# Performance work log

Hardware: AMD Instinct MI355X
Metric: run time of the kernel (lower is better)

Reference implementation:

```python
import jax, jax.numpy as jnp
import numpy as np

L, D, H, E, K, HID = 4096, 1024, 16, 8, 2, 4096
HEAD_DIM = D // H
SCALE = 1.0 / np.sqrt(HEAD_DIM)


def setup_inputs() -> dict:
    key = jax.random.key(0)
    ks = jax.random.split(key, 9)
    s = 0.02
    return {
        "Q": jax.random.normal(ks[0], (L, D), dtype=jnp.float32),
        "K": jax.random.normal(ks[1], (L, D), dtype=jnp.float32),
        "V": jax.random.normal(ks[2], (L, D), dtype=jnp.float32),
        "gate_w": jax.random.normal(ks[3], (D, E), dtype=jnp.float32) * s,
        "w1": jax.random.normal(ks[4], (E, D, HID), dtype=jnp.float32) * s,
        "b1": jnp.zeros((E, HID), dtype=jnp.float32),
        "w2": jax.random.normal(ks[5], (E, HID, D), dtype=jnp.float32) * s,
        "b2": jnp.zeros((E, D), dtype=jnp.float32),
    }


def attention(Q, Kt, V):
    # [L, D] -> [L, H, head_dim]
    q = Q.reshape(L, H, HEAD_DIM)
    k = Kt.reshape(L, H, HEAD_DIM)
    v = V.reshape(L, H, HEAD_DIM)
    scores = jnp.einsum("qhd,khd->hqk", q, k) * SCALE  # [H, L, L]
    probs = jax.nn.softmax(scores, axis=-1)
    out = jnp.einsum("hqk,khd->qhd", probs, v)  # [L, H, head_dim]
    return out.reshape(L, D)


def moe(x, gate_w, w1, b1, w2, b2):
    # x: [N, D]; top-k gating with softmax over selected logits
    logits = x @ gate_w  # [N, E]
    topv, topi = jax.lax.top_k(logits, K)  # [N, K]
    topw = jax.nn.softmax(topv, axis=-1)
    rows = jnp.arange(x.shape[0])[:, None]
    full_w = jnp.zeros_like(logits).at[rows, topi].set(topw)  # [N, E]
    # dense-masked expert compute (mathematically identical: zero weights kill
    # unrouted tokens). GELU is exact (erf), matching torch nn.GELU default.
    h = jax.nn.gelu(jnp.einsum("nd,edh->enh", x, w1) + b1[:, None, :],
                    approximate=False)  # [E, N, HID]
    y = jnp.einsum("enh,ehd->end", h, w2) + b2[:, None, :]  # [E, N, D]
    return jnp.einsum("ne,end->nd", full_w, y)  # weighted combine


def reference(Q, K, V, gate_w, w1, b1, w2, b2):
    attn_out = attention(Q, K, V)              # [L, D]
    out = moe(attn_out, gate_w, w1, b1, w2, b2)  # [L, D]
    return out
```

## Files before the change

kernel.cpp:

```cpp
#include <hip/hip_runtime.h>
#include <hip/hip_bf16.h>
#include <math.h>

#define L_SEQ 4096
#define DMODEL 1024
#define NHEAD 16
#define HDIM 64
#define NEXP 8
#define NHID 4096
#define NSLOT (L_SEQ * 2)

typedef __attribute__((ext_vector_type(4))) float f32x4;
typedef __attribute__((ext_vector_type(16))) float f32x16;
typedef __attribute__((ext_vector_type(8))) short s16x8;
typedef __attribute__((ext_vector_type(4))) short s16x4;
typedef __attribute__((ext_vector_type(4))) unsigned u32x4;

__device__ __forceinline__ short f2bf(float f) {
  __hip_bfloat16 h = __float2bfloat16(f);
  return *reinterpret_cast<short*>(&h);
}
__device__ __forceinline__ float bf2f(short s) {
  __hip_bfloat16 h;
  *reinterpret_cast<short*>(&h) = s;
  return __bfloat162float(h);
}
__device__ __forceinline__ void split3(float a, short& h, short& m, short& l) {
  h = f2bf(a);
  float r = a - bf2f(h);
  m = f2bf(r);
  float r2 = r - bf2f(m);
  l = f2bf(r2);
}
__device__ __forceinline__ void gload16(const void* g, void* l) {
  __builtin_amdgcn_global_load_lds(
      (const __attribute__((address_space(1))) void*)g,
      (__attribute__((address_space(3))) void*)l, 16, 0, 0);
}

__global__ __launch_bounds__(256) void split_kernel(const float* __restrict__ src,
                                                    short* __restrict__ hs,
                                                    short* __restrict__ ms,
                                                    short* __restrict__ ls,
                                                    float scale, int nquad) {
  int i = blockIdx.x * 256 + threadIdx.x;
  for (; i < nquad; i += gridDim.x * 256) {
    f32x4 a = reinterpret_cast<const f32x4*>(src)[i];
    a *= scale;
    s16x4 h4, m4, l4;
    #pragma unroll
    for (int j = 0; j < 4; ++j) {
      short h, m, l;
      split3(a[j], h, m, l);
      h4[j] = h; m4[j] = m; l4[j] = l;
    }
    reinterpret_cast<s16x4*>(hs)[i] = h4;
    reinterpret_cast<s16x4*>(ms)[i] = m4;
    reinterpret_cast<s16x4*>(ls)[i] = l4;
  }
}

__global__ __launch_bounds__(256) void split_vt_kernel(const float* __restrict__ V,
                                                       short* __restrict__ Vth,
                                                       short* __restrict__ Vtm,
                                                       short* __restrict__ Vtl) {
  __shared__ float Vlds[64][65];
  const int k0 = blockIdx.x * 64;
  const int head = blockIdx.y;
  const int t = threadIdx.x;
  {
    int r = t >> 2, c = (t & 3) * 16;
    const f32x4* src = reinterpret_cast<const f32x4*>(&V[(size_t)(k0 + r) * DMODEL + head * HDIM + c]);
    #pragma unroll
    for (int j = 0; j < 4; ++j)
      *reinterpret_cast<f32x4*>(&Vlds[r][c + 4 * j]) = src[j];
  }
  __syncthreads();
  {
    int d = t >> 2, kc = (t & 3) * 16;
    s16x8 h8[2], m8[2], l8[2];
    #pragma unroll
    for (int j = 0; j < 16; ++j) {
      float v = Vlds[kc + j][d];
      short h, m, l;
      split3(v, h, m, l);
      h8[j >> 3][j & 7] = h; m8[j >> 3][j & 7] = m; l8[j >> 3][j & 7] = l;
    }
    size_t base = (size_t)(head * HDIM + d) * L_SEQ + k0 + kc;
    *reinterpret_cast<s16x8*>(&Vth[base]) = h8[0];
    *reinterpret_cast<s16x8*>(&Vth[base + 8]) = h8[1];
    *reinterpret_cast<s16x8*>(&Vtm[base]) = m8[0];
    *reinterpret_cast<s16x8*>(&Vtm[base + 8]) = m8[1];
    *reinterpret_cast<s16x8*>(&Vtl[base]) = l8[0];
    *reinterpret_cast<s16x8*>(&Vtl[base + 8]) = l8[1];
  }
}

__global__ __launch_bounds__(256) void wtrans_kernel(const float* __restrict__ src,
                                                     short* __restrict__ dst,
                                                     int R, int C) {
  __shared__ float T[64][65];
  const int e = blockIdx.z;
  const int r0 = blockIdx.y * 64, c0 = blockIdx.x * 64;
  const size_t sbase = (size_t)e * R * C;
  const int t = threadIdx.x;
  {
    int rr = t >> 2, cc = (t & 3) * 16;
    #pragma unroll
    for (int j = 0; j < 4; ++j)
      *reinterpret_cast<f32x4*>(&T[rr][cc + 4 * j]) =
          *reinterpret_cast<const f32x4*>(&src[sbase + (size_t)(r0 + rr) * C + c0 + cc + 4 * j]);
  }
  __syncthreads();
  {
    int c = t >> 2, r = (t & 3) * 16;
    s16x8 v0, v1;
    #pragma unroll
    for (int j = 0; j < 8; ++j) { v0[j] = f2bf(T[r + j][c]); v1[j] = f2bf(T[r + 8 + j][c]); }
    size_t dbase = ((size_t)e * C + c0 + c) * R + r0 + r;
    *reinterpret_cast<s16x8*>(&dst[dbase]) = v0;
    *reinterpret_cast<s16x8*>(&dst[dbase + 8]) = v1;
  }
}

__global__ __launch_bounds__(256, 2) void attn_mfma(
    const short* __restrict__ Qh, const short* __restrict__ Qm, const short* __restrict__ Ql,
    const short* __restrict__ Kh, const short* __restrict__ Km, const short* __restrict__ Kl,
    const short* __restrict__ Vth, const short* __restrict__ Vtm, const short* __restrict__ Vtl,
    float* __restrict__ X, short* __restrict__ Xb) {
  __shared__ short Ks[3][64][70];
  __shared__ short Vs[3][64][70];
  const int lin = blockIdx.x;
  const int swz = (lin & 7) * 64 + (lin >> 3);
  const int head = swz >> 5;
  const int q0 = (swz & 31) << 7;
  const int t = threadIdx.x;
  const int l = t & 63;
  const int wq = t >> 6;
  const int lc = l & 31;
  const int hh = l >> 5;

  const short* Qp[3] = {Qh, Qm, Ql};
  const short* Kp[3] = {Kh, Km, Kl};
  const short* Vp[3] = {Vth, Vtm, Vtl};

  s16x8 qf[3][4];
  {
    size_t qrow = (size_t)(q0 + wq * 32 + lc) * DMODEL + head * HDIM;
    #pragma unroll
    for (int s = 0; s < 3; ++s)
      #pragma unroll
      for (int ds_ = 0; ds_ < 4; ++ds_)
        qf[s][ds_] = *reinterpret_cast<const s16x8*>(&Qp[s][qrow + ds_ * 16 + hh * 8]);
  }

  s16x8 sK[3][2], sV[3][2];
  const int c0 = t * 2;
  const int row0 = c0 >> 3, ch0 = (c0 & 7) * 8;
  const int row1 = (c0 + 1) >> 3, ch1 = ((c0 + 1) & 7) * 8;

  #define LOAD_TILE(k0v)                                                                  \
    _Pragma("unroll")                                                                     \
    for (int s = 0; s < 3; ++s) {                                                         \
      sK[s][0] = *reinterpret_cast<const s16x8*>(&Kp[s][(size_t)((k0v) + row0) * DMODEL + head * HDIM + ch0]); \
      sK[s][1] = *reinterpret_cast<const s16x8*>(&Kp[s][(size_t)((k0v) + row1) * DMODEL + head * HDIM + ch1]); \
      sV[s][0] = *reinterpret_cast<const s16x8*>(&Vp[s][(size_t)(head * HDIM + row0) * L_SEQ + (k0v) + ch0]);  \
      sV[s][1] = *reinterpret_cast<const s16x8*>(&Vp[s][(size_t)(head * HDIM + row1) * L_SEQ + (k0v) + ch1]);  \
    }

  f32x16 acc0 = (f32x16)0.f, acc1 = (f32x16)0.f;
  float l_loc = 0.f;
  const float LOG2E = 1.4426950408889634f;
  const float MBIAS = 46.166241f;

  LOAD_TILE(0);

  for (int kt64 = 0; kt64 < 64; ++kt64) {
    __syncthreads();
    #pragma unroll
    for (int s = 0; s < 3; ++s) {
      *reinterpret_cast<s16x8*>(&Ks[s][row0][ch0]) = sK[s][0];
      *reinterpret_cast<s16x8*>(&Ks[s][row1][ch1]) = sK[s][1];
      *reinterpret_cast<s16x8*>(&Vs[s][row0][ch0]) = sV[s][0];
      *reinterpret_cast<s16x8*>(&Vs[s][row1][ch1]) = sV[s][1];
    }
    __syncthreads();
    if (kt64 < 63) { LOAD_TILE((kt64 + 1) * 64); }

    #pragma unroll
    for (int khalf = 0; khalf < 2; ++khalf) {
      f32x16 st = (f32x16)0.f;
      #pragma unroll
      for (int ds_ = 0; ds_ < 4; ++ds_) {
        s16x8 ah = *reinterpret_cast<const s16x8*>(&Ks[0][khalf * 32 + lc][ds_ * 16 + hh * 8]);
        s16x8 am = *reinterpret_cast<const s16x8*>(&Ks[1][khalf * 32 + lc][ds_ * 16 + hh * 8]);
        s16x8 al = *reinterpret_cast<const s16x8*>(&Ks[2][khalf * 32 + lc][ds_ * 16 + hh * 8]);
        st = __builtin_amdgcn_mfma_f32_32x32x16_bf16(am, qf[1][ds_], st, 0, 0, 0);
        st = __builtin_amdgcn_mfma_f32_32x32x16_bf16(al, qf[0][ds_], st, 0, 0, 0);
        st = __builtin_amdgcn_mfma_f32_32x32x16_bf16(ah, qf[2][ds_], st, 0, 0, 0);
        st = __builtin_amdgcn_mfma_f32_32x32x16_bf16(am, qf[0][ds_], st, 0, 0, 0);
        st = __builtin_amdgcn_mfma_f32_32x32x16_bf16(ah, qf[1][ds_], st, 0, 0, 0);
        st = __builtin_amdgcn_mfma_f32_32x32x16_bf16(ah, qf[0][ds_], st, 0, 0, 0);
      }

      unsigned Eh[4][2], Em[4][2], El[4][2];
      float ps = 0.f;
      #pragma unroll
      for (int q = 0; q < 4; ++q) {
        #pragma unroll
        for (int p = 0; p < 2; ++p) {
          float a = exp2f(fmaf(st[4 * q + 2 * p],     LOG2E, -MBIAS));
          float b = exp2f(fmaf(st[4 * q + 2 * p + 1], LOG2E, -MBIAS));
          ps += a + b;
          unsigned ua = __float_as_uint(a), ub = __float_as_uint(b);
          unsigned ha = ua & 0xffff0000u, hb = ub & 0xffff0000u;
          Eh[q][p] = (ha >> 16) | hb;
          float ra = a - __uint_as_float(ha), rb = b - __uint_as_float(hb);
          unsigned ma = __float_as_uint(ra) & 0xffff0000u, mb = __float_as_uint(rb) & 0xffff0000u;
          Em[q][p] = (ma >> 16) | mb;
          float la = ra - __uint_as_float(ma), lb = rb - __uint_as_float(mb);
          El[q][p] = ((__float_as_uint(la) & 0xffff0000u) >> 16) | (__float_as_uint(lb) & 0xffff0000u);
        }
      }
      l_loc += ps;

      #define EXCH(E, Fout) do { u32x4 f_;                                        \
        _Pragma("unroll") for (int p_ = 0; p_ < 2; ++p_) {                        \
          unsigned sel_ = hh ? E[2 * ks][p_] : E[2 * ks + 1][p_];                 \
          unsigned rc_ = (unsigned)__shfl_xor((int)sel_, 32);                     \
          f_[p_] = hh ? rc_ : E[2 * ks][p_];                                      \
          f_[2 + p_] = hh ? E[2 * ks + 1][p_] : rc_;                              \
        }                                                                         \
        Fout = *reinterpret_cast<s16x8*>(&f_); } while (0)

      #pragma unroll
      for (int ks = 0; ks < 2; ++ks) {
        s16x8 Fh, Fm, Fl;
        EXCH(Eh, Fh);
        EXCH(Em, Fm);
        EXCH(El, Fl);
        const int kcol = khalf * 32 + ks * 16 + hh * 8;
        {
          s16x8 vh = *reinterpret_cast<const s16x8*>(&Vs[0][lc][kcol]);
          s16x8 vm = *reinterpret_cast<const s16x8*>(&Vs[1][lc][kcol]);
          s16x8 vl = *reinterpret_cast<const s16x8*>(&Vs[2][lc][kcol]);
          acc0 = __builtin_amdgcn_mfma_f32_32x32x16_bf16(Fm, vm, acc0, 0, 0, 0);
          acc0 = __builtin_amdgcn_mfma_f32_32x32x16_bf16(Fl, vh, acc0, 0, 0, 0);
          acc0 = __builtin_amdgcn_mfma_f32_32x32x16_bf16(Fh, vl, acc0, 0, 0, 0);
          acc0 = __builtin_amdgcn_mfma_f32_32x32x16_bf16(Fm, vh, acc0, 0, 0, 0);
          acc0 = __builtin_amdgcn_mfma_f32_32x32x16_bf16(Fh, vm, acc0, 0, 0, 0);
          acc0 = __builtin_amdgcn_mfma_f32_32x32x16_bf16(Fh, vh, acc0, 0, 0, 0);
        }
        {
          s16x8 vh = *reinterpret_cast<const s16x8*>(&Vs[0][32 + lc][kcol]);
          s16x8 vm = *reinterpret_cast<const s16x8*>(&Vs[1][32 + lc][kcol]);
          s16x8 vl = *reinterpret_cast<const s16x8*>(&Vs[2][32 + lc][kcol]);
          acc1 = __builtin_amdgcn_mfma_f32_32x32x16_bf16(Fm, vm, acc1, 0, 0, 0);
          acc1 = __builtin_amdgcn_mfma_f32_32x32x16_bf16(Fl, vh, acc1, 0, 0, 0);
          acc1 = __builtin_amdgcn_mfma_f32_32x32x16_bf16(Fh, vl, acc1, 0, 0, 0);
          acc1 = __builtin_amdgcn_mfma_f32_32x32x16_bf16(Fm, vh, acc1, 0, 0, 0);
          acc1 = __builtin_amdgcn_mfma_f32_32x32x16_bf16(Fh, vm, acc1, 0, 0, 0);
          acc1 = __builtin_amdgcn_mfma_f32_32x32x16_bf16(Fh, vh, acc1, 0, 0, 0);
        }
      }
      #undef EXCH
    }
  }

  float l_tot = l_loc + __shfl_xor(l_loc, 32);
  float inv = 1.f / l_tot;
  #pragma unroll
  for (int r = 0; r < 16; ++r) {
    int qrow_ = (r & 3) + 8 * (r >> 2) + 4 * hh;
    float invr = __int_as_float(__builtin_amdgcn_ds_bpermute(qrow_ << 2, __float_as_int(inv)));
    size_t base = (size_t)(q0 + wq * 32 + qrow_) * DMODEL + head * HDIM + lc;
    float o0 = acc0[r] * invr, o1 = acc1[r] * invr;
    X[base] = o0;
    X[base + 32] = o1;
    Xb[base] = f2bf(o0);
    Xb[base + 32] = f2bf(o1);
  }
}

__global__ __launch_bounds__(256) void gate_kernel(const float* __restrict__ X,
                                                   const float* __restrict__ GW,
                                                   int* __restrict__ tokE,
                                                   float* __restrict__ tokW,
                                                   int* __restrict__ meta) {
  const int gid = blockIdx.x * 256 + threadIdx.x;
  const int n = gid >> 6;
  const int lane = threadIdx.x & 63;
  double lacc[8];
  #pragma unroll
  for (int e = 0; e < 8; ++e) lacc[e] = 0.0;
  #pragma unroll
  for (int ch = 0; ch < 4; ++ch) {
    int d0 = ch * 256 + lane * 4;
    f32x4 xv = *reinterpret_cast<const f32x4*>(&X[(size_t)n * DMODEL + d0]);
    #pragma unroll
    for (int j = 0; j < 4; ++j) {
      const f32x4* g = reinterpret_cast<const f32x4*>(&GW[(size_t)(d0 + j) * 8]);
      f32x4 g0 = g[0], g1 = g[1];
      double xd = (double)xv[j];
      lacc[0] += xd * (double)g0[0]; lacc[1] += xd * (double)g0[1];
      lacc[2] += xd * (double)g0[2]; lacc[3] += xd * (double)g0[3];
      lacc[4] += xd * (double)g1[0]; lacc[5] += xd * (double)g1[1];
      lacc[6] += xd * (double)g1[2]; lacc[7] += xd * (double)g1[3];
    }
  }
  #pragma unroll
  for (int e = 0; e < 8; ++e) {
    double v = lacc[e];
    #pragma unroll
    for (int off = 32; off > 0; off >>= 1) v += __shfl_down(v, off);
    lacc[e] = v;
  }
  if (lane == 0) {
    float lg[8];
    #pragma unroll
    for (int e = 0; e < 8; ++e) lg[e] = (float)lacc[e];
    int i0 = 0;
    for (int e = 1; e < 8; ++e) if (lg[e] > lg[i0]) i0 = e;
    int i1 = -1;
    for (int e = 0; e < 8; ++e) {
      if (e == i0) continue;
      if (i1 < 0 || lg[e] > lg[i1]) i1 = e;
    }
    float eb = expf(lg[i1] - lg[i0]);
    float wa = 1.f / (1.f + eb);
    float wb = eb * wa;
    tokE[2 * n] = i0; tokE[2 * n + 1] = i1;
    tokW[2 * n] = wa; tokW[2 * n + 1] = wb;
    atomicAdd(&meta[i0], 1);
    atomicAdd(&meta[i1], 1);
  }
}

__global__ void scan_kernel(int* meta) {
  if (threadIdx.x == 0) {
    int s = 0;
    for (int e = 0; e < 8; ++e) { meta[8 + e] = s; meta[16 + e] = s; s += meta[e]; }
  }
}

__global__ __launch_bounds__(256) void assign_kernel(const int* __restrict__ tokE,
                                                     const float* __restrict__ tokW,
                                                     int* __restrict__ meta,
                                                     int* __restrict__ list,
                                                     float* __restrict__ wl) {
  int n = blockIdx.x * 256 + threadIdx.x;
  if (n >= L_SEQ) return;
  #pragma unroll
  for (int k2 = 0; k2 < 2; ++k2) {
    int e = tokE[2 * n + k2];
    int slot = atomicAdd(&meta[16 + e], 1);
    list[slot] = n;
    wl[slot] = tokW[2 * n + k2];
  }
}

__global__ __launch_bounds__(256) void gemm1p_kernel(const short* __restrict__ Xb,
                                                     const short* __restrict__ W1t,
                                                     const float* __restrict__ B1,
                                                     const int* __restrict__ meta,
                                                     const int* __restrict__ list,
                                                     short* __restrict__ Hb) {
  const int e = blockIdx.z;
  const int cntE = meta[e];
  const int flat = blockIdx.x + gridDim.x * blockIdx.y;
  const int xcd = flat & 7;
  const int idx = flat >> 3;
  const int m0 = (idx & 31) << 7;
  const int n0 = ((xcd << 2) + (idx >> 5)) << 7;
  if (m0 >= cntE) return;
  const int baseE = meta[8 + e];

  __shared__ short As[3][128 * 32];
  __shared__ short Bs[3][128 * 32];

  const int t = threadIdx.x;
  const int l = t & 63;
  const int w = t >> 6;
  const int wm = w >> 1, wn = w & 1;
  const int ln = l & 15, kg = l >> 4;

  size_t asrc[2], bsrc[2];
  #pragma unroll
  for (int c = 0; c < 2; ++c) {
    int idx2 = c * 256 + t;
    int row = idx2 >> 2;
    int sch = (idx2 & 3) ^ ((row >> 2) & 3);
    int idxm = m0 + row; if (idxm > cntE - 1) idxm = cntE - 1;
    int grow = list[baseE + idxm];
    asrc[c] = ((size_t)grow * DMODEL + sch * 8) * 2;
    bsrc[c] = (((size_t)e * NHID + n0 + row) * DMODEL + sch * 8) * 2;
  }

  f32x4 acc[4][4];
  #pragma unroll
  for (int mi = 0; mi < 4; ++mi)
    #pragma unroll
    for (int ni = 0; ni < 4; ++ni) acc[mi][ni] = (f32x4)0.f;

  #define STG1(h_, bf_) do { size_t ko_ = (size_t)(h_) * 64;                        \
    _Pragma("unroll")                                                               \
    for (int c_ = 0; c_ < 2; ++c_) {                                                \
      gload16((const char*)Xb + asrc[c_] + ko_, (char*)As + (bf_) * 8192 + c_ * 4096 + t * 16);  \
      gload16((const char*)W1t + bsrc[c_] + ko_, (char*)Bs + (bf_) * 8192 + c_ * 4096 + t * 16); \
    } } while (0)

  const int H = DMODEL / 32;
  STG1(0, 0); STG1(1, 1);
  for (int h = 0; h < H; ++h) {
    if (h < H - 1) asm volatile("s_waitcnt vmcnt(4)\ns_barrier" ::: "memory");
    else           asm volatile("s_waitcnt vmcnt(0)\ns_barrier" ::: "memory");
    if (h + 2 < H) STG1(h + 2, (h + 2) % 3);
    const char* ab = (const char*)As + (h % 3) * 8192;
    const char* bb = (const char*)Bs + (h % 3) * 8192;
    s16x8 af[4];
    #pragma unroll
    for (int mi = 0; mi < 4; ++mi) {
      int row = wm * 64 + mi * 16 + ln;
      int cc = kg ^ ((row >> 2) & 3);
      af[mi] = *reinterpret_cast<const s16x8*>(ab + row * 64 + cc * 16);
    }
    #pragma unroll
    for (int ni = 0; ni < 4; ++ni) {
      int col = wn * 64 + ni * 16 + ln;
      int cc = kg ^ ((col >> 2) & 3);
      s16x8 bfr = *reinterpret_cast<const s16x8*>(bb + col * 64 + cc * 16);
      #pragma unroll
      for (int mi = 0; mi < 4; ++mi)
        acc[mi][ni] = __builtin_amdgcn_mfma_f32_16x16x32_bf16(af[mi], bfr, acc[mi][ni], 0, 0, 0);
    }
  }

  #pragma unroll
  for (int mi = 0; mi < 4; ++mi) {
    #pragma unroll
    for (int r = 0; r < 4; ++r) {
      int rl = wm * 64 + mi * 16 + kg * 4 + r;
      if (m0 + rl >= cntE) continue;
      size_t hrow = (size_t)(baseE + m0 + rl) * NHID;
      #pragma unroll
      for (int ni = 0; ni < 4; ++ni) {
        int col = n0 + wn * 64 + ni * 16 + ln;
        float z = acc[mi][ni][r] + B1[e * NHID + col];
        float g = 0.5f * z * (1.f + erff(z * 0.70710678118f));
        Hb[hrow + col] = f2bf(g);
      }
    }
  }
}

__global__ __launch_bounds__(256) void gemm2p_kernel(const short* __restrict__ Hb,
                                                     const short* __restrict__ W2t,
                                                     const float* __restrict__ B2,
                                                     const int* __restrict__ meta,
                                                     const int* __restrict__ list,
                                                     const float* __restrict__ wl,
                                                     float* __restrict__ out) {
  const int e = blockIdx.z;
  const int cntE = meta[e];
  const int flat = blockIdx.x + gridDim.x * blockIdx.y;
  const int m0 = (flat >> 3) << 7;
  const int n0 = (flat & 7) << 7;
  if (m0 >= cntE) return;
  const int baseE = meta[8 + e];

  __shared__ short As[3][128 * 32];
  __shared__ short Bs[3][128 * 32];

  const int t = threadIdx.x;
  const int l = t & 63;
  const int w = t >> 6;
  const int wm = w >> 1, wn = w & 1;
  const int ln = l & 15, kg = l >> 4;

  size_t asrc[2], bsrc[2];
  #pragma unroll
  for (int c = 0; c < 2; ++c) {
    int idx2 = c * 256 + t;
    int row = idx2 >> 2;
    int sch = (idx2 & 3) ^ ((row >> 2) & 3);
    int idxm = m0 + row; if (idxm > cntE - 1) idxm = cntE - 1;
    asrc[c] = (((size_t)(baseE + idxm)) * NHID + sch * 8) * 2;
    bsrc[c] = (((size_t)e * DMODEL + n0 + row) * NHID + sch * 8) * 2;
  }

  f32x4 acc[4][4];
  #pragma unroll
  for (int mi = 0; mi < 4; ++mi)
    #pragma unroll
    for (int ni = 0; ni < 4; ++ni) acc[mi][ni] = (f32x4)0.f;

  #define STG2(h_, bf_) do { size_t ko_ = (size_t)(h_) * 64;                        \
    _Pragma("unroll")                                                               \
    for (int c_ = 0; c_ < 2; ++c_) {                                                \
      gload16((const char*)Hb + asrc[c_] + ko_, (char*)As + (bf_) * 8192 + c_ * 4096 + t * 16);  \
      gload16((const char*)W2t + bsrc[c_] + ko_, (char*)Bs + (bf_) * 8192 + c_ * 4096 + t * 16); \
    } } while (0)

  const int H = NHID / 32;
  STG2(0, 0); STG2(1, 1);
  for (int h = 0; h < H; ++h) {
    if (h < H - 1) asm volatile("s_waitcnt vmcnt(4)\ns_barrier" ::: "memory");
    else           asm volatile("s_waitcnt vmcnt(0)\ns_barrier" ::: "memory");
    if (h + 2 < H) STG2(h + 2, (h + 2) % 3);
    const char* ab = (const char*)As + (h % 3) * 8192;
    const char* bb = (const char*)Bs + (h % 3) * 8192;
    s16x8 af[4];
    #pragma unroll
    for (int mi = 0; mi < 4; ++mi) {
      int row = wm * 64 + mi * 16 + ln;
      int cc = kg ^ ((row >> 2) & 3);
      af[mi] = *reinterpret_cast<const s16x8*>(ab + row * 64 + cc * 16);
    }
    #pragma unroll
    for (int ni = 0; ni < 4; ++ni) {
      int col = wn * 64 + ni * 16 + ln;
      int cc = kg ^ ((col >> 2) & 3);
      s16x8 bfr = *reinterpret_cast<const s16x8*>(bb + col * 64 + cc * 16);
      #pragma unroll
      for (int mi = 0; mi < 4; ++mi)
        acc[mi][ni] = __builtin_amdgcn_mfma_f32_16x16x32_bf16(af[mi], bfr, acc[mi][ni], 0, 0, 0);
    }
  }

  #pragma unroll
  for (int mi = 0; mi < 4; ++mi) {
    #pragma unroll
    for (int r = 0; r < 4; ++r) {
      int rl = wm * 64 + mi * 16 + kg * 4 + r;
      if (m0 + rl >= cntE) continue;
      int slot = baseE + m0 + rl;
      int token = list[slot];
      float wgt = wl[slot];
      #pragma unroll
      for (int ni = 0; ni < 4; ++ni) {
        int col = n0 + wn * 64 + ni * 16 + ln;
        float z = acc[mi][ni][r] + B2[e * DMODEL + col];
        atomicAdd(&out[(size_t)token * DMODEL + col], wgt * z);
      }
    }
  }
}

extern "C" void kernel_launch(void* const* d_in, const int* in_sizes, int n_in,
                              void* d_out, int out_size, void* d_ws, size_t ws_size,
                              hipStream_t stream) {
  const float* Q  = (const float*)d_in[0];
  const float* K  = (const float*)d_in[1];
  const float* V  = (const float*)d_in[2];
  const float* GW = (const float*)d_in[3];
  const float* W1 = (const float*)d_in[4];
  const float* B1 = (const float*)d_in[5];
  const float* W2 = (const float*)d_in[6];
  const float* B2 = (const float*)d_in[7];
  float* out = (float*)d_out;

  const size_t SPLIT = (size_t)L_SEQ * DMODEL;
  const size_t WT_BYTES = (size_t)NEXP * NHID * DMODEL * 2;
  const size_t SPLIT_REGION = SPLIT * 2 * 9;
  const size_t SMALL = (size_t)L_SEQ * 2 * 4 * 2 + (size_t)NSLOT * 4 * 2 + 256;
  const size_t PRIMARY_BYTES = WT_BYTES * 2 + SPLIT_REGION + SPLIT * 4 + SPLIT * 2 + SMALL;
  if (ws_size < PRIMARY_BYTES) return;

  char* ws = (char*)d_ws;
  const int nquad = (int)(SPLIT / 4);

  size_t off = 0;
  short* W1t = (short*)(ws + off); off += WT_BYTES;
  short* W2t = (short*)(ws + off); off += WT_BYTES;
  char*  splits = ws + off;        off += SPLIT_REGION;
  short* Qh = (short*)(splits);
  short* Qm = Qh + SPLIT;  short* Ql = Qm + SPLIT;
  short* Kh = Ql + SPLIT;  short* Km = Kh + SPLIT;  short* Kl = Km + SPLIT;
  short* Vth = Kl + SPLIT; short* Vtm = Vth + SPLIT; short* Vtl = Vtm + SPLIT;
  short* Hb = (short*)splits;
  float* Xf = (float*)(ws + off);  off += SPLIT * 4;
  short* Xb = (short*)(ws + off);  off += SPLIT * 2;
  int*   tokE = (int*)(ws + off);  off += (size_t)L_SEQ * 2 * 4;
  float* tokW = (float*)(ws + off); off += (size_t)L_SEQ * 2 * 4;
  int*   list = (int*)(ws + off);  off += (size_t)NSLOT * 4;
  float* wl = (float*)(ws + off);  off += (size_t)NSLOT * 4;
  int*   meta = (int*)(ws + off);  off += 256;

  hipMemsetAsync(out, 0, (size_t)out_size * sizeof(float), stream);
  hipMemsetAsync(meta, 0, 256, stream);

  wtrans_kernel<<<dim3(64, 16, 8), 256, 0, stream>>>(W1, W1t, DMODEL, NHID);
  wtrans_kernel<<<dim3(16, 64, 8), 256, 0, stream>>>(W2, W2t, NHID, DMODEL);
  split_kernel<<<dim3(2048), 256, 0, stream>>>(Q, Qh, Qm, Ql, 0.125f, nquad);
  split_kernel<<<dim3(2048), 256, 0, stream>>>(K, Kh, Km, Kl, 1.0f, nquad);
  split_vt_kernel<<<dim3(64, 16), 256, 0, stream>>>(V, Vth, Vtm, Vtl);
  attn_mfma<<<dim3(512), 256, 0, stream>>>(Qh, Qm, Ql, Kh, Km, Kl, Vth, Vtm, Vtl, Xf, Xb);
  gate_kernel<<<dim3(1024), 256, 0, stream>>>(Xf, GW, tokE, tokW, meta);
  scan_kernel<<<1, 64, 0, stream>>>(meta);
  assign_kernel<<<dim3(16), 256, 0, stream>>>(tokE, tokW, meta, list, wl);
  gemm1p_kernel<<<dim3(32, 32, 8), 256, 0, stream>>>(Xb, W1t, B1, meta, list, Hb);
  gemm2p_kernel<<<dim3(32, 8, 8), 256, 0, stream>>>(Hb, W2t, B2, meta, list, wl, out);
}
```

Measured before the change: 992.3 us.

## Fuse prep kernels, compact MoE grids via tile maps, enlarge GEMM1 M-tile

Result: slower. 1.105 ms (+11.3%).

```diff
diff --git a/kernel.cpp b/kernel.cpp
--- a/kernel.cpp
+++ b/kernel.cpp
@@ -38,70 +38,82 @@
       (__attribute__((address_space(3))) void*)l, 16, 0, 0);
 }
 
-__global__ __launch_bounds__(256) void split_kernel(const float* __restrict__ src,
-                                                    short* __restrict__ hs,
-                                                    short* __restrict__ ms,
-                                                    short* __restrict__ ls,
-                                                    float scale, int nquad) {
-  int i = blockIdx.x * 256 + threadIdx.x;
-  for (; i < nquad; i += gridDim.x * 256) {
-    f32x4 a = reinterpret_cast<const f32x4*>(src)[i];
-    a *= scale;
-    s16x4 h4, m4, l4;
-    #pragma unroll
-    for (int j = 0; j < 4; ++j) {
-      short h, m, l;
-      split3(a[j], h, m, l);
-      h4[j] = h; m4[j] = m; l4[j] = l;
-    }
-    reinterpret_cast<s16x4*>(hs)[i] = h4;
-    reinterpret_cast<s16x4*>(ms)[i] = m4;
-    reinterpret_cast<s16x4*>(ls)[i] = l4;
-  }
-}
-
-__global__ __launch_bounds__(256) void split_vt_kernel(const float* __restrict__ V,
-                                                       short* __restrict__ Vth,
-                                                       short* __restrict__ Vtm,
-                                                       short* __restrict__ Vtl) {
+__global__ __launch_bounds__(256) void prep_kernel(
+    const float* __restrict__ Q, const float* __restrict__ K, const float* __restrict__ V,
+    short* __restrict__ Qh, short* __restrict__ Qm, short* __restrict__ Ql,
+    short* __restrict__ Kh, short* __restrict__ Km, short* __restrict__ Kl,
+    short* __restrict__ Vth, short* __restrict__ Vtm, short* __restrict__ Vtl) {
   __shared__ float Vlds[64][65];
-  const int k0 = blockIdx.x * 64;
-  const int head = blockIdx.y;
+  const int b = blockIdx.x;
   const int t = threadIdx.x;
-  {
-    int r = t >> 2, c = (t & 3) * 16;
-    const f32x4* src = reinterpret_cast<const f32x4*>(&V[(size_t)(k0 + r) * DMODEL + head * HDIM + c]);
-    #pragma unroll
-    for (int j = 0; j < 4; ++j)
-      *reinterpret_cast<f32x4*>(&Vlds[r][c + 4 * j]) = src[j];
-  }
-  __syncthreads();
-  {
-    int d = t >> 2, kc = (t & 3) * 16;
-    s16x8 h8[2], m8[2], l8[2];
-    #pragma unroll
-    for (int j = 0; j < 16; ++j) {
-      float v = Vlds[kc + j][d];
-      short h, m, l;
-      split3(v, h, m, l);
-      h8[j >> 3][j & 7] = h; m8[j >> 3][j & 7] = m; l8[j >> 3][j & 7] = l;
-    }
-    size_t base = (size_t)(head * HDIM + d) * L_SEQ + k0 + kc;
-    *reinterpret_cast<s16x8*>(&Vth[base]) = h8[0];
-    *reinterpret_cast<s16x8*>(&Vth[base + 8]) = h8[1];
-    *reinterpret_cast<s16x8*>(&Vtm[base]) = m8[0];
-    *reinterpret_cast<s16x8*>(&Vtm[base + 8]) = m8[1];
-    *reinterpret_cast<s16x8*>(&Vtl[base]) = l8[0];
-    *reinterpret_cast<s16x8*>(&Vtl[base + 8]) = l8[1];
-  }
-}
-
-__global__ __launch_bounds__(256) void wtrans_kernel(const float* __restrict__ src,
-                                                     short* __restrict__ dst,
-                                                     int R, int C) {
+  if (b < 4096) {
+    const bool isQ = (b < 2048);
+    const float* src = isQ ? Q : K;
+    short* hs = isQ ? Qh : Kh;
+    short* ms = isQ ? Qm : Km;
+    short* ls = isQ ? Ql : Kl;
+    const float scale = isQ ? 0.125f : 1.0f;
+    const int nquad = (int)((size_t)L_SEQ * DMODEL / 4);
+    int i = (b & 2047) * 256 + t;
+    for (; i < nquad; i += 2048 * 256) {
+      f32x4 a = reinterpret_cast<const f32x4*>(src)[i];
+      a *= scale;
+      s16x4 h4, m4, l4;
+      #pragma unroll
+      for (int j = 0; j < 4; ++j) {
+        short h, m, l;
+        split3(a[j], h, m, l);
+        h4[j] = h; m4[j] = m; l4[j] = l;
+      }
+      reinterpret_cast<s16x4*>(hs)[i] = h4;
+      reinterpret_cast<s16x4*>(ms)[i] = m4;
+      reinterpret_cast<s16x4*>(ls)[i] = l4;
+    }
+  } else {
+    const int b2 = b - 4096;
+    const int k0 = (b2 & 63) * 64;
+    const int head = b2 >> 6;
+    {
+      int r = t >> 2, c = (t & 3) * 16;
+      const f32x4* src = reinterpret_cast<const f32x4*>(&V[(size_t)(k0 + r) * DMODEL + head * HDIM + c]);
+      #pragma unroll
+      for (int j = 0; j < 4; ++j)
+        *reinterpret_cast<f32x4*>(&Vlds[r][c + 4 * j]) = src[j];
+    }
+    __syncthreads();
+    {
+      int d = t >> 2, kc = (t & 3) * 16;
+      s16x8 h8[2], m8[2], l8[2];
+      #pragma unroll
+      for (int j = 0; j < 16; ++j) {
+        float v = Vlds[kc + j][d];
+        short h, m, l;
+        split3(v, h, m, l);
+        h8[j >> 3][j & 7] = h; m8[j >> 3][j & 7] = m; l8[j >> 3][j & 7] = l;
+      }
+      size_t base = (size_t)(head * HDIM + d) * L_SEQ + k0 + kc;
+      *reinterpret_cast<s16x8*>(&Vth[base]) = h8[0];
+      *reinterpret_cast<s16x8*>(&Vth[base + 8]) = h8[1];
+      *reinterpret_cast<s16x8*>(&Vtm[base]) = m8[0];
+      *reinterpret_cast<s16x8*>(&Vtm[base + 8]) = m8[1];
+      *reinterpret_cast<s16x8*>(&Vtl[base]) = l8[0];
+      *reinterpret_cast<s16x8*>(&Vtl[base + 8]) = l8[1];
+    }
+  }
+}
+
+__global__ __launch_bounds__(256) void wtrans_kernel(const float* __restrict__ W1,
+                                                     const float* __restrict__ W2,
+                                                     short* __restrict__ W1t,
+                                                     short* __restrict__ W2t) {
   __shared__ float T[64][65];
-  const int e = blockIdx.z;
-  const int r0 = blockIdx.y * 64, c0 = blockIdx.x * 64;
+  const int f = blockIdx.x;
+  const int z = blockIdx.y;
+  const float* src;
+  short* dst;
+  int R, C, r0, c0, e;
+  if (z < 8) { e = z; R = DMODEL; C = NHID; src = W1; dst = W1t; r0 = (f >> 6) * 64; c0 = (f & 63) * 64; }
+  else { e = z - 8; R = NHID; C = DMODEL; src = W2; dst = W2t; r0 = (f >> 4) * 64; c0 = (f & 15) * 64; }
   const size_t sbase = (size_t)e * R * C;
   const int t = threadIdx.x;
   {
@@ -336,10 +348,18 @@
   }
 }
 
-__global__ void scan_kernel(int* meta) {
+__global__ void scan_kernel(int* meta, int* map1, int* map2) {
   if (threadIdx.x == 0) {
-    int s = 0;
-    for (int e = 0; e < 8; ++e) { meta[8 + e] = s; meta[16 + e] = s; s += meta[e]; }
+    int s = 0, c1 = 0, c2 = 0;
+    for (int e = 0; e < 8; ++e) {
+      meta[8 + e] = s; meta[16 + e] = s;
+      int cnt = meta[e];
+      for (int m0 = 0; m0 < cnt; m0 += 256) { map1[2 * c1] = e; map1[2 * c1 + 1] = m0; ++c1; }
+      for (int m0 = 0; m0 < cnt; m0 += 128) { map2[2 * c2] = e; map2[2 * c2 + 1] = m0; ++c2; }
+      s += cnt;
+    }
+    for (; c1 < 64; ++c1) map1[2 * c1] = -1;
+    for (; c2 < 80; ++c2) map2[2 * c2] = -1;
   }
 }
 
@@ -359,23 +379,21 @@
   }
 }
 
-__global__ __launch_bounds__(256) void gemm1p_kernel(const short* __restrict__ Xb,
-                                                     const short* __restrict__ W1t,
-                                                     const float* __restrict__ B1,
-                                                     const int* __restrict__ meta,
-                                                     const int* __restrict__ list,
-                                                     short* __restrict__ Hb) {
-  const int e = blockIdx.z;
+__global__ __launch_bounds__(256, 2) void gemm1p_kernel(const short* __restrict__ Xb,
+                                                        const short* __restrict__ W1t,
+                                                        const float* __restrict__ B1,
+                                                        const int* __restrict__ meta,
+                                                        const int* __restrict__ list,
+                                                        const int* __restrict__ map1,
+                                                        short* __restrict__ Hb) {
+  const int e = map1[2 * blockIdx.x];
+  if (e < 0) return;
+  const int m0 = map1[2 * blockIdx.x + 1];
+  const int n0 = blockIdx.y << 7;
   const int cntE = meta[e];
-  const int flat = blockIdx.x + gridDim.x * blockIdx.y;
-  const int xcd = flat & 7;
-  const int idx = flat >> 3;
-  const int m0 = (idx & 31) << 7;
-  const int n0 = ((xcd << 2) + (idx >> 5)) << 7;
-  if (m0 >= cntE) return;
   const int baseE = meta[8 + e];
 
-  __shared__ short As[3][128 * 32];
+  __shared__ short As[3][256 * 32];
   __shared__ short Bs[3][128 * 32];
 
   const int t = threadIdx.x;
@@ -384,62 +402,70 @@
   const int wm = w >> 1, wn = w & 1;
   const int ln = l & 15, kg = l >> 4;
 
-  size_t asrc[2], bsrc[2];
-  #pragma unroll
-  for (int c = 0; c < 2; ++c) {
+  size_t asrc[4], bsrc[2];
+  #pragma unroll
+  for (int c = 0; c < 4; ++c) {
     int idx2 = c * 256 + t;
     int row = idx2 >> 2;
     int sch = (idx2 & 3) ^ ((row >> 2) & 3);
     int idxm = m0 + row; if (idxm > cntE - 1) idxm = cntE - 1;
     int grow = list[baseE + idxm];
     asrc[c] = ((size_t)grow * DMODEL + sch * 8) * 2;
+  }
+  #pragma unroll
+  for (int c = 0; c < 2; ++c) {
+    int idx2 = c * 256 + t;
+    int row = idx2 >> 2;
+    int sch = (idx2 & 3) ^ ((row >> 2) & 3);
     bsrc[c] = (((size_t)e * NHID + n0 + row) * DMODEL + sch * 8) * 2;
   }
 
-  f32x4 acc[4][4];
-  #pragma unroll
-  for (int mi = 0; mi < 4; ++mi)
+  f32x4 acc[8][4];
+  #pragma unroll
+  for (int mi = 0; mi < 8; ++mi)
     #pragma unroll
     for (int ni = 0; ni < 4; ++ni) acc[mi][ni] = (f32x4)0.f;
 
   #define STG1(h_, bf_) do { size_t ko_ = (size_t)(h_) * 64;                        \
     _Pragma("unroll")                                                               \
-    for (int c_ = 0; c_ < 2; ++c_) {                                                \
-      gload16((const char*)Xb + asrc[c_] + ko_, (char*)As + (bf_) * 8192 + c_ * 4096 + t * 16);  \
+    for (int c_ = 0; c_ < 4; ++c_)                                                  \
+      gload16((const char*)Xb + asrc[c_] + ko_, (char*)As + (bf_) * 16384 + c_ * 4096 + t * 16); \
+    _Pragma("unroll")                                                               \
+    for (int c_ = 0; c_ < 2; ++c_)                                                  \
       gload16((const char*)W1t + bsrc[c_] + ko_, (char*)Bs + (bf_) * 8192 + c_ * 4096 + t * 16); \
-    } } while (0)
+    } while (0)
 
   const int H = DMODEL / 32;
   STG1(0, 0); STG1(1, 1);
   for (int h = 0; h < H; ++h) {
-    if (h < H - 1) asm volatile("s_waitcnt vmcnt(4)\ns_barrier" ::: "memory");
+    if (h < H - 1) asm volatile("s_waitcnt vmcnt(6)\ns_barrier" ::: "memory");
     else           asm volatile("s_waitcnt vmcnt(0)\ns_barrier" ::: "memory");
     if (h + 2 < H) STG1(h + 2, (h + 2) % 3);
-    const char* ab = (const char*)As + (h % 3) * 8192;
+    const char* ab = (const char*)As + (h % 3) * 16384;
     const char* bb = (const char*)Bs + (h % 3) * 8192;
-    s16x8 af[4];
-    #pragma unroll
-    for (int mi = 0; mi < 4; ++mi) {
-      int row = wm * 64 + mi * 16 + ln;
-      int cc = kg ^ ((row >> 2) & 3);
-      af[mi] = *reinterpret_cast<const s16x8*>(ab + row * 64 + cc * 16);
-    }
+    s16x8 bf[4];
     #pragma unroll
     for (int ni = 0; ni < 4; ++ni) {
       int col = wn * 64 + ni * 16 + ln;
       int cc = kg ^ ((col >> 2) & 3);
-      s16x8 bfr = *reinterpret_cast<const s16x8*>(bb + col * 64 + cc * 16);
-      #pragma unroll
-      for (int mi = 0; mi < 4; ++mi)
-        acc[mi][ni] = __builtin_amdgcn_mfma_f32_16x16x32_bf16(af[mi], bfr, acc[mi][ni], 0, 0, 0);
-    }
-  }
-
-  #pragma unroll
-  for (int mi = 0; mi < 4; ++mi) {
+      bf[ni] = *reinterpret_cast<const s16x8*>(bb + col * 64 + cc * 16);
+    }
+    #pragma unroll
+    for (int mi = 0; mi < 8; ++mi) {
+      int row = wm * 128 + mi * 16 + ln;
+      int cc = kg ^ ((row >> 2) & 3);
+      s16x8 af = *reinterpret_cast<const s16x8*>(ab + row * 64 + cc * 16);
+      #pragma unroll
+      for (int ni = 0; ni < 4; ++ni)
+        acc[mi][ni] = __builtin_amdgcn_mfma_f32_16x16x32_bf16(af, bf[ni], acc[mi][ni], 0, 0, 0);
+    }
+  }
+
+  #pragma unroll
+  for (int mi = 0; mi < 8; ++mi) {
     #pragma unroll
     for (int r = 0; r < 4; ++r) {
-      int rl = wm * 64 + mi * 16 + kg * 4 + r;
+      int rl = wm * 128 + mi * 16 + kg * 4 + r;
       if (m0 + rl >= cntE) continue;
       size_t hrow = (size_t)(baseE + m0 + rl) * NHID;
       #pragma unroll
@@ -459,13 +485,13 @@
                                                      const int* __restrict__ meta,
                                                      const int* __restrict__ list,
                                                      const float* __restrict__ wl,
+                                                     const int* __restrict__ map2,
                                                      float* __restrict__ out) {
-  const int e = blockIdx.z;
+  const int e = map2[2 * blockIdx.x];
+  if (e < 0) return;
+  const int m0 = map2[2 * blockIdx.x + 1];
+  const int n0 = blockIdx.y << 7;
   const int cntE = meta[e];
-  const int flat = blockIdx.x + gridDim.x * blockIdx.y;
-  const int m0 = (flat >> 3) << 7;
-  const int n0 = (flat & 7) << 7;
-  if (m0 >= cntE) return;
   const int baseE = meta[8 + e];
 
   __shared__ short As[3][128 * 32];
@@ -562,12 +588,11 @@
   const size_t SPLIT = (size_t)L_SEQ * DMODEL;
   const size_t WT_BYTES = (size_t)NEXP * NHID * DMODEL * 2;
   const size_t SPLIT_REGION = SPLIT * 2 * 9;
-  const size_t SMALL = (size_t)L_SEQ * 2 * 4 * 2 + (size_t)NSLOT * 4 * 2 + 256;
+  const size_t SMALL = (size_t)L_SEQ * 2 * 4 * 2 + (size_t)NSLOT * 4 * 2 + 4096;
   const size_t PRIMARY_BYTES = WT_BYTES * 2 + SPLIT_REGION + SPLIT * 4 + SPLIT * 2 + SMALL;
   if (ws_size < PRIMARY_BYTES) return;
 
   char* ws = (char*)d_ws;
-  const int nquad = (int)(SPLIT / 4);
 
   size_t off = 0;
   short* W1t = (short*)(ws + off); off += WT_BYTES;
@@ -585,19 +610,18 @@
   int*   list = (int*)(ws + off);  off += (size_t)NSLOT * 4;
   float* wl = (float*)(ws + off);  off += (size_t)NSLOT * 4;
   int*   meta = (int*)(ws + off);  off += 256;
+  int*   map1 = (int*)(ws + off);  off += 64 * 2 * 4;
+  int*   map2 = (int*)(ws + off);  off += 80 * 2 * 4;
 
   hipMemsetAsync(out, 0, (size_t)out_size * sizeof(float), stream);
   hipMemsetAsync(meta, 0, 256, stream);
 
-  wtrans_kernel<<<dim3(64, 16, 8), 256, 0, stream>>>(W1, W1t, DMODEL, NHID);
-  wtrans_kernel<<<dim3(16, 64, 8), 256, 0, stream>>>(W2, W2t, NHID, DMODEL);
-  split_kernel<<<dim3(2048), 256, 0, stream>>>(Q, Qh, Qm, Ql, 0.125f, nquad);
-  split_kernel<<<dim3(2048), 256, 0, stream>>>(K, Kh, Km, Kl, 1.0f, nquad);
-  split_vt_kernel<<<dim3(64, 16), 256, 0, stream>>>(V, Vth, Vtm, Vtl);
+  wtrans_kernel<<<dim3(1024, 16), 256, 0, stream>>>(W1, W2, W1t, W2t);
+  prep_kernel<<<dim3(5120), 256, 0, stream>>>(Q, K, V, Qh, Qm, Ql, Kh, Km, Kl, Vth, Vtm, Vtl);
   attn_mfma<<<dim3(512), 256, 0, stream>>>(Qh, Qm, Ql, Kh, Km, Kl, Vth, Vtm, Vtl, Xf, Xb);
   gate_kernel<<<dim3(1024), 256, 0, stream>>>(Xf, GW, tokE, tokW, meta);
-  scan_kernel<<<1, 64, 0, stream>>>(meta);
+  scan_kernel<<<1, 64, 0, stream>>>(meta, map1, map2);
   assign_kernel<<<dim3(16), 256, 0, stream>>>(tokE, tokW, meta, list, wl);
-  gemm1p_kernel<<<dim3(32, 32, 8), 256, 0, stream>>>(Xb, W1t, B1, meta, list, Hb);
-  gemm2p_kernel<<<dim3(32, 8, 8), 256, 0, stream>>>(Hb, W2t, B2, meta, list, wl, out);
-}
+  gemm1p_kernel<<<dim3(64, 32), 256, 0, stream>>>(Xb, W1t, B1, meta, list, map1, Hb);
+  gemm2p_kernel<<<dim3(80, 8), 256, 0, stream>>>(Hb, W2t, B2, meta, list, wl, map2, out);
+}
```
